# Kernel tuning notes

Hardware: AMD Instinct MI355X
Metric: run time of the kernel (lower is better)

## Reference

```python
import jax, jax.numpy as jnp
import numpy as np

ITEMNUM = 50000
NUM_HEADS = 4
EPS = 1e-8


def _ln(x, g, b):
    m = x.mean(-1, keepdims=True)
    v = ((x - m) ** 2).mean(-1, keepdims=True)
    return (x - m) * jax.lax.rsqrt(v + EPS) * g + b


def _forward(seqs_data, position, seqs, time_emb, pos_table, gate_W, gate_b,
             ln_attn_g, ln_attn_b, qW, qb, kW, kb, vW, vb,
             ln_ffn_g, ln_ffn_b, c1W, c1b, c2W, c2b, last_g, last_b):
    B, L, H = seqs.shape
    nb = qW.shape[0]
    hd = H // NUM_HEADS

    pe = pos_table[position]                      # [B,L,H]
    seqs = seqs + pe
    time = time_emb + pe
    # per-position per-block time gates, [B,L,nb]
    gates = jax.nn.sigmoid(jnp.einsum('blh,nh->bln', time, gate_W) + gate_b)

    keep = (seqs_data != ITEMNUM - 1)[..., None].astype(seqs.dtype)  # [B,L,1]
    seqs = seqs * keep
    tril = jnp.tril(jnp.ones((L, L), dtype=bool))  # causal: keep lower triangle
    neg_inf = jnp.asarray(-jnp.inf, seqs.dtype)
    scale = 1.0 / np.sqrt(hd).astype(np.float32)

    for i in range(nb):
        Q = _ln(seqs, ln_attn_g[i], ln_attn_b[i])
        q = Q @ qW[i].T + qb[i]
        k = time @ kW[i].T + kb[i]
        v = (seqs + time) @ vW[i].T + vb[i]
        # [B,nh,L,hd]
        q = q.reshape(B, L, NUM_HEADS, hd).transpose(0, 2, 1, 3)
        k = k.reshape(B, L, NUM_HEADS, hd).transpose(0, 2, 1, 3)
        v = v.reshape(B, L, NUM_HEADS, hd).transpose(0, 2, 1, 3)
        scores = jnp.einsum('bhqd,bhkd->bhqk', q, k) * scale  # [B,nh,L,L]
        tg = gates[:, :, i]                                   # [B,L]
        gate_mat = tg[:, None, :, None] * tg[:, None, None, :]  # [B,1,L,L] outer product
        scores = jnp.where(tril[None, None], scores * gate_mat, neg_inf)
        attn = jax.nn.softmax(scores, axis=-1)
        out = jnp.einsum('bhqk,bhkd->bhqd', attn, v)
        out = out.transpose(0, 2, 1, 3).reshape(B, L, H)
        x = Q + out
        x = _ln(x, ln_ffn_g[i], ln_ffn_b[i])
        # PointWiseFeedForward: two 1x1 convs == two linears, relu, residual
        h = jax.nn.relu(x @ c1W[i].T + c1b[i])
        seqs = (h @ c2W[i].T + c2b[i] + x) * keep

    return _ln(seqs, last_g, last_b)


def setup_inputs() -> dict:
    key = jax.random.key(0)
    B, L, H, NB, ML = 64, 512, 256, 2, 512
    ks = iter(jax.random.split(key, 32))
    nrm = lambda shape, s=0.05: jax.random.normal(next(ks), shape, jnp.float32) * s
    pos_table = nrm((ML, H), 0.02).at[0].set(0.0)  # padding_idx=0
    inp = {
        'seqs_data': jax.random.randint(next(ks), (B, L), 0, ITEMNUM - 1, jnp.int32),
        'seqs': nrm((B, L, H), 1.0),
        'position': jax.random.randint(next(ks), (B, L), 0, ML, jnp.int32),
        'time_emb': nrm((B, L, H), 1.0),
        'pos_table': pos_table,
        'gate_W': nrm((NB, H)), 'gate_b': jnp.zeros((NB,), jnp.float32),
        'ln_attn_g': jnp.ones((NB, H), jnp.float32), 'ln_attn_b': jnp.zeros((NB, H), jnp.float32),
        'qW': nrm((NB, H, H)), 'qb': jnp.zeros((NB, H), jnp.float32),
        'kW': nrm((NB, H, H)), 'kb': jnp.zeros((NB, H), jnp.float32),
        'vW': nrm((NB, H, H)), 'vb': jnp.zeros((NB, H), jnp.float32),
        'ln_ffn_g': jnp.ones((NB, H), jnp.float32), 'ln_ffn_b': jnp.zeros((NB, H), jnp.float32),
        'c1W': nrm((NB, H, H)), 'c1b': jnp.zeros((NB, H), jnp.float32),
        'c2W': nrm((NB, H, H)), 'c2b': jnp.zeros((NB, H), jnp.float32),
        'last_g': jnp.ones((H,), jnp.float32), 'last_b': jnp.zeros((H,), jnp.float32),
    }
    return inp


def reference(seqs_data, seqs, position, time_emb, pos_table, gate_W, gate_b,
              ln_attn_g, ln_attn_b, qW, qb, kW, kb, vW, vb,
              ln_ffn_g, ln_ffn_b, c1W, c1b, c2W, c2b, last_g, last_b):
    return _forward(seqs_data, position, seqs, time_emb, pos_table, gate_W, gate_b,
                    ln_attn_g, ln_attn_b, qW, qb, kW, kb, vW, vb,
                    ln_ffn_g, ln_ffn_b, c1W, c1b, c2W, c2b, last_g, last_b)
```

## Files before the change

kernel.cpp:

```cpp
#include <hip/hip_runtime.h>
#include <hip/hip_bf16.h>
#include <math.h>

#define NTOK 32768
#define Hdim 256
#define Ldim 512
#define Bdim 64
#define NHEAD 4
#define HD 64
#define PADV 49999

typedef __bf16 bf16x8 __attribute__((ext_vector_type(8)));
typedef __bf16 bf16x4 __attribute__((ext_vector_type(4)));
typedef float  f32x4  __attribute__((ext_vector_type(4)));
typedef unsigned short u16x8 __attribute__((ext_vector_type(8)));

union bf8u { bf16x8 v8; bf16x4 v4[2]; };

__device__ __forceinline__ unsigned short f2bf(float f) {
    unsigned int u = __float_as_uint(f);
    unsigned int r = (u + 0x7fffu + ((u >> 16) & 1u)) >> 16;
    return (unsigned short)r;
}
__device__ __forceinline__ float bf2f(unsigned short u) {
    return __uint_as_float(((unsigned int)u) << 16);
}

__device__ __forceinline__ void gload16(const void* g, void* l) {
    __builtin_amdgcn_global_load_lds((const __attribute__((address_space(1))) unsigned int*)g,
                                     (__attribute__((address_space(3))) unsigned int*)l,
                                     16, 0, 0);
}

__global__ __launch_bounds__(256)
void castw_kernel(const float* __restrict__ q, const float* __restrict__ k,
                  const float* __restrict__ v, const float* __restrict__ c1,
                  const float* __restrict__ c2, unsigned short* __restrict__ dst) {
    const float* srcs[5] = {q, k, v, c1, c2};
    const float* s = srcs[blockIdx.y];
    int idx = blockIdx.x * 1024 + threadIdx.x * 4;
    float4 f = *(const float4*)(s + idx);
    unsigned short* d = dst + (size_t)blockIdx.y * 131072 + idx;
    d[0] = f2bf(f.x); d[1] = f2bf(f.y); d[2] = f2bf(f.z); d[3] = f2bf(f.w);
}

__global__ __launch_bounds__(256)
void prep_ln_kernel(const int* __restrict__ seqs_data, const float* __restrict__ seqs,
                    const int* __restrict__ position, const float* __restrict__ time_emb,
                    const float* __restrict__ pos_table, const float* __restrict__ gate_W,
                    const float* __restrict__ gate_b,
                    const float* __restrict__ lnG, const float* __restrict__ lnB,
                    unsigned short* __restrict__ Tbf,
                    unsigned short* __restrict__ QXbf,
                    unsigned short* __restrict__ VINbf,
                    float* __restrict__ gates, float* __restrict__ keepv) {
    int tok  = blockIdx.x * 4 + (threadIdx.x >> 6);
    int lane = threadIdx.x & 63;
    size_t off = (size_t)tok * Hdim + lane * 4;
    int pos = position[tok];
    float4 pe = *(const float4*)(pos_table + (size_t)pos * Hdim + lane * 4);
    float4 sq = *(const float4*)(seqs + off);
    float4 tm = *(const float4*)(time_emb + off);
    float keep = (seqs_data[tok] != PADV) ? 1.0f : 0.0f;
    float4 t = {tm.x + pe.x, tm.y + pe.y, tm.z + pe.z, tm.w + pe.w};
    float4 s = {(sq.x + pe.x) * keep, (sq.y + pe.y) * keep,
                (sq.z + pe.z) * keep, (sq.w + pe.w) * keep};
    ushort4 tb = {f2bf(t.x), f2bf(t.y), f2bf(t.z), f2bf(t.w)};
    *(ushort4*)(Tbf + off) = tb;
    float4 gw0 = *(const float4*)(gate_W + lane * 4);
    float4 gw1 = *(const float4*)(gate_W + Hdim + lane * 4);
    float r0 = s.x + s.y + s.z + s.w;
    float r1 = s.x * s.x + s.y * s.y + s.z * s.z + s.w * s.w;
    float r2 = t.x * gw0.x + t.y * gw0.y + t.z * gw0.z + t.w * gw0.w;
    float r3 = t.x * gw1.x + t.y * gw1.y + t.z * gw1.z + t.w * gw1.w;
#pragma unroll
    for (int o = 1; o < 64; o <<= 1) {
        r0 += __shfl_xor(r0, o, 64);
        r1 += __shfl_xor(r1, o, 64);
        r2 += __shfl_xor(r2, o, 64);
        r3 += __shfl_xor(r3, o, 64);
    }
    float mean = r0 * (1.0f / Hdim);
    float var  = fmaxf(r1 * (1.0f / Hdim) - mean * mean, 0.0f);
    float rstd = rsqrtf(var + 1e-8f);
    if (lane == 0) {
        gates[(size_t)tok * 2 + 0] = 1.0f / (1.0f + __expf(-(r2 + gate_b[0])));
        gates[(size_t)tok * 2 + 1] = 1.0f / (1.0f + __expf(-(r3 + gate_b[1])));
        keepv[tok] = keep;
    }
    float4 g4 = *(const float4*)(lnG + lane * 4);
    float4 b4 = *(const float4*)(lnB + lane * 4);
    float4 y = {(s.x - mean) * rstd * g4.x + b4.x, (s.y - mean) * rstd * g4.y + b4.y,
                (s.z - mean) * rstd * g4.z + b4.z, (s.w - mean) * rstd * g4.w + b4.w};
    ushort4 yb = {f2bf(y.x), f2bf(y.y), f2bf(y.z), f2bf(y.w)};
    *(ushort4*)(QXbf + off) = yb;
    ushort4 vb = {f2bf(s.x + t.x), f2bf(s.y + t.y), f2bf(s.z + t.z), f2bf(s.w + t.w)};
    *(ushort4*)(VINbf + off) = vb;
}

#define GBM 128
#define GBN 128
#define GBK 64

__device__ __forceinline__ void stage64(const unsigned short* __restrict__ src,
                                        size_t rowBase, __bf16* lds, int tid, int kc) {
#pragma unroll
    for (int it = 0; it < 4; ++it) {
        int c = tid + it * 256;
        int r = c >> 3, sub = c & 7;
        int g = sub ^ (r & 7);
        gload16(src + (rowBase + r) * Hdim + kc + g * 8, lds + c * 8);
    }
}
__device__ __forceinline__ bf16x8 frag64(const __bf16* lds, int r, int g) {
    return *(const bf16x8*)(lds + r * 64 + (g ^ (r & 7)) * 8);
}

__global__ __launch_bounds__(256)
void gemm_qkv_kernel(const unsigned short* __restrict__ QXbf,
                     const unsigned short* __restrict__ Tbf,
                     const unsigned short* __restrict__ VINbf,
                     const unsigned short* __restrict__ qW,
                     const unsigned short* __restrict__ kW,
                     const unsigned short* __restrict__ vW,
                     const float* __restrict__ qb, const float* __restrict__ kb,
                     const float* __restrict__ vb,
                     unsigned short* __restrict__ Qbf,
                     unsigned short* __restrict__ Kbf,
                     unsigned short* __restrict__ VT) {
    __shared__ __align__(16) char smem[128 * 136 * 2];
    __bf16* As = (__bf16*)smem;
    __bf16* Ws = (__bf16*)(smem + 16384);
    __bf16 (*Ct)[136] = (__bf16 (*)[136])smem;
    int z = blockIdx.z;
    const unsigned short* A = (z == 0) ? QXbf : (z == 1) ? Tbf : VINbf;
    const unsigned short* W = (z == 0) ? qW : (z == 1) ? kW : vW;
    const float* bias       = (z == 0) ? qb : (z == 1) ? kb : vb;

    int tid = threadIdx.x, lane = tid & 63, w = tid >> 6;
    int wr = w >> 1, wc = w & 1;
    int m0 = blockIdx.y * GBM, n0 = blockIdx.x * GBN;
    f32x4 acc[4][4];
#pragma unroll
    for (int i = 0; i < 4; ++i)
#pragma unroll
        for (int j = 0; j < 4; ++j) acc[i][j] = (f32x4)(0.0f);
    int colq = lane & 15, kg = lane >> 4;
    for (int kc = 0; kc < Hdim; kc += GBK) {
        __syncthreads();
        stage64(A, m0, As, tid, kc);
        stage64(W, n0, Ws, tid, kc);
        __syncthreads();
        bf16x8 af[4][2], bfr[4][2];
#pragma unroll
        for (int i = 0; i < 4; ++i) {
            int r = wr * 64 + i * 16 + colq;
            af[i][0] = frag64(As, r, kg);
            af[i][1] = frag64(As, r, 4 + kg);
        }
#pragma unroll
        for (int j = 0; j < 4; ++j) {
            int r = wc * 64 + j * 16 + colq;
            bfr[j][0] = frag64(Ws, r, kg);
            bfr[j][1] = frag64(Ws, r, 4 + kg);
        }
#pragma unroll
        for (int i = 0; i < 4; ++i)
#pragma unroll
            for (int j = 0; j < 4; ++j) {
                acc[i][j] = __builtin_amdgcn_mfma_f32_16x16x32_bf16(af[i][0], bfr[j][0], acc[i][j], 0, 0, 0);
                acc[i][j] = __builtin_amdgcn_mfma_f32_16x16x32_bf16(af[i][1], bfr[j][1], acc[i][j], 0, 0, 0);
            }
    }
    int rowq = (lane >> 4) * 4;
    if (z < 2) {
        unsigned short* outBF = (z == 0) ? Qbf : Kbf;
#pragma unroll
        for (int i = 0; i < 4; ++i)
#pragma unroll
            for (int r = 0; r < 4; ++r) {
                int m = m0 + wr * 64 + i * 16 + rowq + r;
#pragma unroll
                for (int j = 0; j < 4; ++j) {
                    int n = n0 + wc * 64 + j * 16 + colq;
                    outBF[(size_t)m * Hdim + n] = f2bf(acc[i][j][r] + bias[n]);
                }
            }
    } else {
        __syncthreads();
#pragma unroll
        for (int i = 0; i < 4; ++i)
#pragma unroll
            for (int r = 0; r < 4; ++r) {
                int ml = wr * 64 + i * 16 + rowq + r;
#pragma unroll
                for (int j = 0; j < 4; ++j) {
                    int nl = wc * 64 + j * 16 + colq;
                    Ct[nl][ml] = (__bf16)(acc[i][j][r] + bias[n0 + nl]);
                }
            }
        __syncthreads();
        int bb = m0 >> 9, l0 = m0 & 511;
#pragma unroll
        for (int it = 0; it < 8; ++it) {
            int c = tid + it * 256;
            int nl = c >> 4;
            int o8 = (c & 15) * 8;
            int n = n0 + nl;
            int hh = n >> 6, dd = n & 63;
            bf16x8 v = *(const bf16x8*)&Ct[nl][o8];
            *(bf16x8*)(VT + ((((size_t)bb * NHEAD + hh) * HD + dd) * Ldim + l0 + o8)) = v;
        }
    }
}

#define FBM 64
#define FFN_LDS (32768 + 32768 + 512)

__device__ __forceinline__ int swz(int r, int g) {
    return (g & 24) | ((g & 7) ^ (r & 7));
}

__device__ __forceinline__ void ffn_stage(const unsigned short* __restrict__ W, int kc,
                                          __bf16* Wst, int tid) {
#pragma unroll
    for (int it = 0; it < 8; ++it) {
        int c = tid + it * 256;
        int r = c >> 3, sub = c & 7;
        int g = sub ^ (r & 7);
        gload16(W + (size_t)r * Hdim + kc + g * 8, Wst + c * 8);
    }
}

__device__ __forceinline__ void ffn_gemm(const unsigned short* __restrict__ W,
                                         const __bf16* Abuf, __bf16* Wst,
                                         int tid, int w, int colq, int kg,
                                         f32x4 acc[4][4]) {
#pragma unroll
    for (int i = 0; i < 4; ++i)
#pragma unroll
        for (int j = 0; j < 4; ++j) acc[i][j] = (f32x4)(0.0f);
    for (int kc = 0; kc < Hdim; kc += 64) {
        __syncthreads();
        bf16x8 af[4][2], bfr[4][2];
#pragma unroll
        for (int i = 0; i < 4; ++i) {
            int r = i * 16 + colq;
            af[i][0] = *(const bf16x8*)(Abuf + r * 256 + ((kc >> 3) | (kg ^ (r & 7))) * 8);
            af[i][1] = *(const bf16x8*)(Abuf + r * 256 + ((kc >> 3) | ((4 + kg) ^ (r & 7))) * 8);
        }
#pragma unroll
        for (int j = 0; j < 4; ++j) {
            int n = w * 64 + j * 16 + colq;
            bfr[j][0] = frag64(Wst, n, kg);
            bfr[j][1] = frag64(Wst, n, 4 + kg);
        }
        __syncthreads();
        if (kc < Hdim - 64) ffn_stage(W, kc + 64, Wst, tid);
#pragma unroll
        for (int i = 0; i < 4; ++i)
#pragma unroll
            for (int j = 0; j < 4; ++j) {
                acc[i][j] = __builtin_amdgcn_mfma_f32_16x16x32_bf16(af[i][0], bfr[j][0], acc[i][j], 0, 0, 0);
                acc[i][j] = __builtin_amdgcn_mfma_f32_16x16x32_bf16(af[i][1], bfr[j][1], acc[i][j], 0, 0, 0);
            }
    }
}

__global__ __launch_bounds__(256, 2)
void ffn_kernel(const unsigned short* __restrict__ Qx,
                const unsigned short* __restrict__ Qa,
                const float* __restrict__ lnG, const float* __restrict__ lnB,
                const unsigned short* __restrict__ c1Wb, const float* __restrict__ c1b,
                const unsigned short* __restrict__ c2Wb, const float* __restrict__ c2b,
                const float* __restrict__ keepv,
                const unsigned short* __restrict__ Tbf,
                const float* __restrict__ oG, const float* __restrict__ oB,
                float* __restrict__ outF,
                unsigned short* __restrict__ QxOut,
                unsigned short* __restrict__ VINout) {
    extern __shared__ __align__(16) char smem[];
    __bf16* Abuf   = (__bf16*)smem;
    __bf16* Wst    = (__bf16*)(smem + 32768);
    float*  statsF = (float*)(smem + 65536);

    int m0  = blockIdx.x * FBM;
    int tid = threadIdx.x, lane = tid & 63, w = tid >> 6;
    int colq = lane & 15, kg = lane >> 4;
    int rowq = kg * 4;

    ffn_stage(c1Wb, 0, Wst, tid);

    u16x8 qvr[8], avr[8];
#pragma unroll
    for (int it = 0; it < 8; ++it) {
        int c = tid + it * 256;
        int r = c >> 5, g = c & 31;
        size_t off = (size_t)(m0 + r) * Hdim + g * 8;
        qvr[it] = *(const u16x8*)(Qx + off);
        avr[it] = *(const u16x8*)(Qa + off);
    }
#pragma unroll
    for (int it = 0; it < 8; ++it) {
        int c = tid + it * 256;
        int r = c >> 5;
        float cs = 0.0f, cq = 0.0f;
#pragma unroll
        for (int j = 0; j < 8; ++j) {
            float x = bf2f(qvr[it][j]) + bf2f(avr[it][j]);
            cs += x; cq += x * x;
        }
#pragma unroll
        for (int o = 1; o < 32; o <<= 1) {
            cs += __shfl_xor(cs, o, 32);
            cq += __shfl_xor(cq, o, 32);
        }
        if ((tid & 31) == 0) { statsF[r * 2] = cs; statsF[r * 2 + 1] = cq; }
    }
    __syncthreads();
    u16x8 xnreg[8];
#pragma unroll
    for (int it = 0; it < 8; ++it) {
        int c = tid + it * 256;
        int r = c >> 5, g = c & 31, col = g * 8;
        float mean = statsF[r * 2] * (1.0f / Hdim);
        float var  = fmaxf(statsF[r * 2 + 1] * (1.0f / Hdim) - mean * mean, 0.0f);
        float rstd = rsqrtf(var + 1e-8f);
        float4 g0 = *(const float4*)(lnG + col), g1 = *(const float4*)(lnG + col + 4);
        float4 b0 = *(const float4*)(lnB + col), b1 = *(const float4*)(lnB + col + 4);
        float gv[8] = {g0.x, g0.y, g0.z, g0.w, g1.x, g1.y, g1.z, g1.w};
        float bv[8] = {b0.x, b0.y, b0.z, b0.w, b1.x, b1.y, b1.z, b1.w};
        u16x8 xn;
#pragma unroll
        for (int j = 0; j < 8; ++j) {
            float x = bf2f(qvr[it][j]) + bf2f(avr[it][j]);
            xn[j] = f2bf((x - mean) * rstd * gv[j] + bv[j]);
        }
        xnreg[it] = xn;
        *(u16x8*)(Abuf + r * 256 + swz(r, g) * 8) = xn;
    }

    f32x4 acc[4][4];
    ffn_gemm(c1Wb, Abuf, Wst, tid, w, colq, kg, acc);
    ffn_stage(c2Wb, 0, Wst, tid);
    float bj[4];
#pragma unroll
    for (int j = 0; j < 4; ++j) bj[j] = c1b[w * 64 + j * 16 + colq];
#pragma unroll
    for (int i = 0; i < 4; ++i)
#pragma unroll
        for (int r = 0; r < 4; ++r) {
            int m = i * 16 + rowq + r;
#pragma unroll
            for (int j = 0; j < 4; ++j) {
                int n = w * 64 + j * 16 + colq;
                float v = fmaxf(acc[i][j][r] + bj[j], 0.0f);
                Abuf[m * 256 + swz(m, n >> 3) * 8 + (n & 7)] = (__bf16)v;
            }
        }

    ffn_gemm(c2Wb, Abuf, Wst, tid, w, colq, kg, acc);
#pragma unroll
    for (int j = 0; j < 4; ++j) bj[j] = c2b[w * 64 + j * 16 + colq];
#pragma unroll
    for (int i = 0; i < 4; ++i)
#pragma unroll
        for (int r = 0; r < 4; ++r) {
            int m = i * 16 + rowq + r;
#pragma unroll
            for (int j = 0; j < 4; ++j) {
                int n = w * 64 + j * 16 + colq;
                Abuf[m * 256 + swz(m, n >> 3) * 8 + (n & 7)] = (__bf16)(acc[i][j][r] + bj[j]);
            }
        }
    __syncthreads();

    u16x8 zvr[8];
#pragma unroll
    for (int it = 0; it < 8; ++it) {
        int c = tid + it * 256;
        int r = c >> 5, g = c & 31;
        zvr[it] = *(const u16x8*)(Abuf + r * 256 + swz(r, g) * 8);
    }
#pragma unroll
    for (int it = 0; it < 8; ++it) {
        int c = tid + it * 256;
        int r = c >> 5;
        float kf = keepv[m0 + r];
        float cs = 0.0f, cq = 0.0f;
#pragma unroll
        for (int j = 0; j < 8; ++j) {
            float s = (bf2f(zvr[it][j]) + bf2f(xnreg[it][j])) * kf;
            cs += s; cq += s * s;
        }
#pragma unroll
        for (int o = 1; o < 32; o <<= 1) {
            cs += __shfl_xor(cs, o, 32);
            cq += __shfl_xor(cq, o, 32);
        }
        if ((tid & 31) == 0) { statsF[r * 2] = cs; statsF[r * 2 + 1] = cq; }
    }
    __syncthreads();
#pragma unroll
    for (int it = 0; it < 8; ++it) {
        int c = tid + it * 256;
        int r = c >> 5, g = c & 31, col = g * 8;
        float kf = keepv[m0 + r];
        float mean = statsF[r * 2] * (1.0f / Hdim);
        float var  = fmaxf(statsF[r * 2 + 1] * (1.0f / Hdim) - mean * mean, 0.0f);
        float rstd = rsqrtf(var + 1e-8f);
        float4 g0 = *(const float4*)(oG + col), g1 = *(const float4*)(oG + col + 4);
        float4 b0 = *(const float4*)(oB + col), b1 = *(const float4*)(oB + col + 4);
        float gv[8] = {g0.x, g0.y, g0.z, g0.w, g1.x, g1.y, g1.z, g1.w};
        float bv[8] = {b0.x, b0.y, b0.z, b0.w, b1.x, b1.y, b1.z, b1.w};
        size_t off = (size_t)(m0 + r) * Hdim + col;
        float y[8], sv[8];
#pragma unroll
        for (int j = 0; j < 8; ++j) {
            sv[j] = (bf2f(zvr[it][j]) + bf2f(xnreg[it][j])) * kf;
            y[j] = (sv[j] - mean) * rstd * gv[j] + bv[j];
        }
        if (outF) {
            float4 o0 = {y[0], y[1], y[2], y[3]};
            float4 o1 = {y[4], y[5], y[6], y[7]};
            *(float4*)(outF + off)     = o0;
            *(float4*)(outF + off + 4) = o1;
        } else {
            u16x8 yb, vb;
            u16x8 tv = *(const u16x8*)(Tbf + off);
#pragma unroll
            for (int j = 0; j < 8; ++j) {
                yb[j] = f2bf(y[j]);
                vb[j] = f2bf(sv[j] + bf2f(tv[j]));
            }
            *(u16x8*)(QxOut + off)  = yb;
            *(u16x8*)(VINout + off) = vb;
        }
    }
}

#define AKS 68
#define AVS 516
#define APS 68
#define ATTN_LDS (512 * AKS * 2 + 64 * AVS * 2 + 192 * APS * 2)
__global__ __launch_bounds__(768, 1)
void attn_mfma_kernel(const unsigned short* __restrict__ Qg,
                      const unsigned short* __restrict__ Kg,
                      const unsigned short* __restrict__ VTg,
                      const float* __restrict__ gates,
                      unsigned short* __restrict__ Ob, int blk) {
    extern __shared__ __align__(16) char smem[];
    __bf16 (*Ks)[AKS]  = (__bf16 (*)[AKS])smem;
    __bf16 (*VTs)[AVS] = (__bf16 (*)[AVS])(smem + 512 * AKS * 2);
    __bf16 (*Ps)[APS]  = (__bf16 (*)[APS])(smem + 512 * AKS * 2 + 64 * AVS * 2);
    int h = blockIdx.x & 3, b = blockIdx.x >> 2;
    int tid = threadIdx.x, lane = tid & 63, w = tid >> 6;
    int colq = lane & 15, grp = lane >> 4;
    int rowq = grp * 4, kq = grp * 8;

    size_t baseK = (size_t)b * Ldim * Hdim + h * HD;
    for (int c = tid; c < 4096; c += 768) {
        int r = c >> 3, o = (c & 7) * 8;
        bf8u u;
        u.v8 = *(const bf16x8*)(Kg + baseK + (size_t)r * Hdim + o);
        *(bf16x4*)&Ks[r][o]     = u.v4[0];
        *(bf16x4*)&Ks[r][o + 4] = u.v4[1];
    }
    size_t baseV = ((size_t)b * NHEAD + h) * HD * Ldim;
    for (int c = tid; c < 4096; c += 768) {
        int d = c >> 6, k = (c & 63) * 8;
        bf8u u;
        u.v8 = *(const bf16x8*)(VTg + baseV + (size_t)d * Ldim + k);
        *(bf16x4*)&VTs[d][k]     = u.v4[0];
        *(bf16x4*)&VTs[d][k + 4] = u.v4[1];
    }
    __syncthreads();

    const float lscale = 0.125f * 1.44269504f;
    int gl[3], ng;
    if (w < 4)      { gl[0] = w;     gl[1] = 8 + w;  gl[2] = 28 + w; ng = 3; }
    else if (w < 8) { gl[0] = w;     gl[1] = 8 + w;  gl[2] = 16 + w; ng = 3; }
    else            { gl[0] = 8 + w; gl[1] = 16 + w; gl[2] = 0;      ng = 2; }

    for (int gi = 0; gi < ng; ++gi) {
        int g = gl[gi];
        int q0 = g * 16;
        size_t qrow = (size_t)(b * Ldim + q0 + colq) * Hdim + h * HD;
        bf16x8 afq0 = *(const bf16x8*)(Qg + qrow + kq);
        bf16x8 afq1 = *(const bf16x8*)(Qg + qrow + 32 + kq);
        float gql[4];
#pragma unroll
        for (int r = 0; r < 4; ++r)
            gql[r] = gates[((size_t)b * Ldim + q0 + rowq + r) * 2 + blk] * lscale;

        float lrun[4] = {0.0f, 0.0f, 0.0f, 0.0f};
        f32x4 accO[4];
#pragma unroll
        for (int jd = 0; jd < 4; ++jd) accO[jd] = (f32x4)(0.0f);

        int nfull = g >> 2;
        for (int kt = 0; kt <= nfull; ++kt) {
            int k0 = kt * 64;
            bool diag = (kt == nfull);
            f32x4 sv[4];
#pragma unroll
            for (int j = 0; j < 4; ++j) sv[j] = (f32x4)(0.0f);
#pragma unroll
            for (int j = 0; j < 4; ++j) {
                int kr = k0 + j * 16 + colq;
                bf8u b0, b1;
                b0.v4[0] = *(const bf16x4*)&Ks[kr][kq];
                b0.v4[1] = *(const bf16x4*)&Ks[kr][kq + 4];
                b1.v4[0] = *(const bf16x4*)&Ks[kr][32 + kq];
                b1.v4[1] = *(const bf16x4*)&Ks[kr][32 + kq + 4];
                sv[j] = __builtin_amdgcn_mfma_f32_16x16x32_bf16(afq0, b0.v8, sv[j], 0, 0, 0);
                sv[j] = __builtin_amdgcn_mfma_f32_16x16x32_bf16(afq1, b1.v8, sv[j], 0, 0, 0);
            }
            float gkv[4];
#pragma unroll
            for (int j = 0; j < 4; ++j)
                gkv[j] = gates[((size_t)b * Ldim + k0 + j * 16 + colq) * 2 + blk];
#pragma unroll
            for (int r = 0; r < 4; ++r) {
                float su = 0.0f;
                float p4[4];
                if (diag) {
                    int qg = q0 + rowq + r;
#pragma unroll
                    for (int j = 0; j < 4; ++j) {
                        float v = sv[j][r] * gql[r] * gkv[j];
                        v = (k0 + j * 16 + colq > qg) ? -1e38f : v;
                        float e = exp2f(v);
                        p4[j] = e;
                        su += e;
                    }
                } else {
#pragma unroll
                    for (int j = 0; j < 4; ++j) {
                        float e = exp2f(sv[j][r] * gql[r] * gkv[j]);
                        p4[j] = e;
                        su += e;
                    }
                }
#pragma unroll
                for (int off = 1; off < 16; off <<= 1)
                    su += __shfl_xor(su, off, 16);
                lrun[r] += su;
#pragma unroll
                for (int j = 0; j < 4; ++j)
                    Ps[w * 16 + rowq + r][j * 16 + colq] = (__bf16)p4[j];
            }
            bf8u a0, a1;
            a0.v4[0] = *(const bf16x4*)&Ps[w * 16 + colq][kq];
            a0.v4[1] = *(const bf16x4*)&Ps[w * 16 + colq][kq + 4];
            a1.v4[0] = *(const bf16x4*)&Ps[w * 16 + colq][32 + kq];
            a1.v4[1] = *(const bf16x4*)&Ps[w * 16 + colq][32 + kq + 4];
#pragma unroll
            for (int jd = 0; jd < 4; ++jd) {
                int vr = jd * 16 + colq;
                bf8u v0, v1;
                v0.v4[0] = *(const bf16x4*)&VTs[vr][k0 + kq];
                v0.v4[1] = *(const bf16x4*)&VTs[vr][k0 + kq + 4];
                v1.v4[0] = *(const bf16x4*)&VTs[vr][k0 + 32 + kq];
                v1.v4[1] = *(const bf16x4*)&VTs[vr][k0 + 32 + kq + 4];
                accO[jd] = __builtin_amdgcn_mfma_f32_16x16x32_bf16(a0.v8, v0.v8, accO[jd], 0, 0, 0);
                accO[jd] = __builtin_amdgcn_mfma_f32_16x16x32_bf16(a1.v8, v1.v8, accO[jd], 0, 0, 0);
            }
        }
#pragma unroll
        for (int r = 0; r < 4; ++r) {
            float inv = 1.0f / lrun[r];
#pragma unroll
            for (int jd = 0; jd < 4; ++jd)
                Ob[(size_t)(b * Ldim + q0 + rowq + r) * Hdim + h * HD + jd * 16 + colq] =
                    f2bf(accO[jd][r] * inv);
        }
    }
}

extern "C" void kernel_launch(void* const* d_in, const int* in_sizes, int n_in,
                              void* d_out, int out_size, void* d_ws, size_t ws_size,
                              hipStream_t stream) {
    const int*   seqs_data = (const int*)d_in[0];
    const float* seqs      = (const float*)d_in[1];
    const int*   position  = (const int*)d_in[2];
    const float* time_emb  = (const float*)d_in[3];
    const float* pos_table = (const float*)d_in[4];
    const float* gate_W    = (const float*)d_in[5];
    const float* gate_b    = (const float*)d_in[6];
    const float* ln_attn_g = (const float*)d_in[7];
    const float* ln_attn_b = (const float*)d_in[8];
    const float* qW        = (const float*)d_in[9];
    const float* qb        = (const float*)d_in[10];
    const float* kW        = (const float*)d_in[11];
    const float* kb        = (const float*)d_in[12];
    const float* vW        = (const float*)d_in[13];
    const float* vb        = (const float*)d_in[14];
    const float* ln_ffn_g  = (const float*)d_in[15];
    const float* ln_ffn_b  = (const float*)d_in[16];
    const float* c1W       = (const float*)d_in[17];
    const float* c1b       = (const float*)d_in[18];
    const float* c2W       = (const float*)d_in[19];
    const float* c2b       = (const float*)d_in[20];
    const float* last_g    = (const float*)d_in[21];
    const float* last_b    = (const float*)d_in[22];

    size_t BUF = (size_t)NTOK * Hdim;
    float* fws = (float*)d_ws;
    float* GATES = fws;
    float* KEEP  = GATES + (size_t)NTOK * 2;
    unsigned short* bws   = (unsigned short*)(KEEP + NTOK);
    unsigned short* Tbf   = bws;
    unsigned short* QXbf  = Tbf + BUF;
    unsigned short* VINbf = QXbf + BUF;
    unsigned short* HIDbf = VINbf + BUF;
    unsigned short* Qbf   = HIDbf + BUF;
    unsigned short* Kbf   = Qbf + BUF;
    unsigned short* VTbf  = Kbf + BUF;
    unsigned short* QAbf  = VTbf + BUF;
    unsigned short* Zbf   = QAbf + BUF;
    unsigned short* Wbf   = Zbf + BUF;
    size_t WB = (size_t)Hdim * Hdim;
    unsigned short* qWbf  = Wbf;
    unsigned short* kWbf  = Wbf + 2 * WB;
    unsigned short* vWbf  = Wbf + 4 * WB;
    unsigned short* c1Wbf = Wbf + 6 * WB;
    unsigned short* c2Wbf = Wbf + 8 * WB;

    castw_kernel<<<dim3(128, 5), 256, 0, stream>>>(qW, kW, vW, c1W, c2W, Wbf);
    prep_ln_kernel<<<NTOK / 4, 256, 0, stream>>>(seqs_data, seqs, position, time_emb,
                                                 pos_table, gate_W, gate_b,
                                                 ln_attn_g, ln_attn_b,
                                                 Tbf, QXbf, VINbf, GATES, KEEP);

    dim3 qkvgrid(Hdim / GBN, NTOK / GBM, 3);
    for (int i = 0; i < 2; ++i) {
        gemm_qkv_kernel<<<qkvgrid, 256, 0, stream>>>(QXbf, Tbf, VINbf,
                                                     qWbf + i * WB, kWbf + i * WB, vWbf + i * WB,
                                                     qb + i * Hdim, kb + i * Hdim, vb + i * Hdim,
                                                     Qbf, Kbf, VTbf);
        attn_mfma_kernel<<<Bdim * NHEAD, 768, ATTN_LDS, stream>>>(Qbf, Kbf, VTbf, GATES, QAbf, i);
        ffn_kernel<<<NTOK / FBM, 256, FFN_LDS, stream>>>(
            QXbf, QAbf,
            ln_ffn_g + i * Hdim, ln_ffn_b + i * Hdim,
            c1Wbf + i * WB, c1b + i * Hdim,
            c2Wbf + i * WB, c2b + i * Hdim,
            KEEP, Tbf,
            (i == 0) ? ln_attn_g + Hdim : last_g,
            (i == 0) ? ln_attn_b + Hdim : last_b,
            (i == 0) ? nullptr : (float*)d_out,
            QXbf, VINbf);
    }
}
```

Before: 357.3 us.

## Stage full FFN weight matrix in LDS and use shuffle-only layernorm stats

The FFN kernel now loads the whole 256x256 bf16 weight matrix (128 KB) into LDS at once instead of streaming 64-column K chunks with per-chunk barriers. The K loop is fully unrolled with no synchronisation inside it. Layernorm statistics come directly from the wave shuffle reduction instead of an LDS round trip and an extra barrier. LDS use grows to about 160 KB per block and the two-blocks-per-CU launch bound is dropped, so occupancy falls to one block per CU and less load latency can be hidden.

```diff
diff --git a/kernel.cpp b/kernel.cpp
--- a/kernel.cpp
+++ b/kernel.cpp
@@ -215,48 +215,48 @@
 }
 
 #define FBM 64
-#define FFN_LDS (32768 + 32768 + 512)
+#define FFN_LDS (32768 + 131072)
 
 __device__ __forceinline__ int swz(int r, int g) {
     return (g & 24) | ((g & 7) ^ (r & 7));
 }
 
-__device__ __forceinline__ void ffn_stage(const unsigned short* __restrict__ W, int kc,
-                                          __bf16* Wst, int tid) {
-#pragma unroll
-    for (int it = 0; it < 8; ++it) {
+__device__ __forceinline__ void ffn_stageW(const unsigned short* __restrict__ W,
+                                           __bf16* Wst, int tid) {
+#pragma unroll
+    for (int it = 0; it < 32; ++it) {
         int c = tid + it * 256;
-        int r = c >> 3, sub = c & 7;
-        int g = sub ^ (r & 7);
-        gload16(W + (size_t)r * Hdim + kc + g * 8, Wst + c * 8);
-    }
-}
-
-__device__ __forceinline__ void ffn_gemm(const unsigned short* __restrict__ W,
-                                         const __bf16* Abuf, __bf16* Wst,
-                                         int tid, int w, int colq, int kg,
-                                         f32x4 acc[4][4]) {
+        int r = c >> 5, s = c & 31;
+        int g = (s & 24) | ((s & 7) ^ (r & 7));
+        gload16(W + (size_t)r * Hdim + g * 8, Wst + c * 8);
+    }
+}
+
+__device__ __forceinline__ bf16x8 fragW(const __bf16* buf, int row, int slot8) {
+    return *(const bf16x8*)(buf + row * 256 + swz(row, slot8) * 8);
+}
+
+__device__ __forceinline__ void ffn_gemm(const __bf16* Abuf, const __bf16* Wst,
+                                         int w, int colq, int kg, f32x4 acc[4][4]) {
 #pragma unroll
     for (int i = 0; i < 4; ++i)
 #pragma unroll
         for (int j = 0; j < 4; ++j) acc[i][j] = (f32x4)(0.0f);
+#pragma unroll
     for (int kc = 0; kc < Hdim; kc += 64) {
-        __syncthreads();
         bf16x8 af[4][2], bfr[4][2];
 #pragma unroll
         for (int i = 0; i < 4; ++i) {
             int r = i * 16 + colq;
-            af[i][0] = *(const bf16x8*)(Abuf + r * 256 + ((kc >> 3) | (kg ^ (r & 7))) * 8);
-            af[i][1] = *(const bf16x8*)(Abuf + r * 256 + ((kc >> 3) | ((4 + kg) ^ (r & 7))) * 8);
+            af[i][0] = fragW(Abuf, r, (kc >> 3) + kg);
+            af[i][1] = fragW(Abuf, r, (kc >> 3) + 4 + kg);
         }
 #pragma unroll
         for (int j = 0; j < 4; ++j) {
             int n = w * 64 + j * 16 + colq;
-            bfr[j][0] = frag64(Wst, n, kg);
-            bfr[j][1] = frag64(Wst, n, 4 + kg);
-        }
-        __syncthreads();
-        if (kc < Hdim - 64) ffn_stage(W, kc + 64, Wst, tid);
+            bfr[j][0] = fragW(Wst, n, (kc >> 3) + kg);
+            bfr[j][1] = fragW(Wst, n, (kc >> 3) + 4 + kg);
+        }
 #pragma unroll
         for (int i = 0; i < 4; ++i)
 #pragma unroll
@@ -267,7 +267,7 @@
     }
 }
 
-__global__ __launch_bounds__(256, 2)
+__global__ __launch_bounds__(256)
 void ffn_kernel(const unsigned short* __restrict__ Qx,
                 const unsigned short* __restrict__ Qa,
                 const float* __restrict__ lnG, const float* __restrict__ lnB,
@@ -280,16 +280,15 @@
                 unsigned short* __restrict__ QxOut,
                 unsigned short* __restrict__ VINout) {
     extern __shared__ __align__(16) char smem[];
-    __bf16* Abuf   = (__bf16*)smem;
-    __bf16* Wst    = (__bf16*)(smem + 32768);
-    float*  statsF = (float*)(smem + 65536);
+    __bf16* Abuf = (__bf16*)smem;
+    __bf16* Wst  = (__bf16*)(smem + 32768);
 
     int m0  = blockIdx.x * FBM;
     int tid = threadIdx.x, lane = tid & 63, w = tid >> 6;
     int colq = lane & 15, kg = lane >> 4;
     int rowq = kg * 4;
 
-    ffn_stage(c1Wb, 0, Wst, tid);
+    ffn_stageW(c1Wb, Wst, tid);
 
     u16x8 qvr[8], avr[8];
 #pragma unroll
@@ -300,31 +299,25 @@
         qvr[it] = *(const u16x8*)(Qx + off);
         avr[it] = *(const u16x8*)(Qa + off);
     }
+    u16x8 xnreg[8];
 #pragma unroll
     for (int it = 0; it < 8; ++it) {
         int c = tid + it * 256;
-        int r = c >> 5;
+        int r = c >> 5, g = c & 31, col = g * 8;
+        float x[8];
         float cs = 0.0f, cq = 0.0f;
 #pragma unroll
         for (int j = 0; j < 8; ++j) {
-            float x = bf2f(qvr[it][j]) + bf2f(avr[it][j]);
-            cs += x; cq += x * x;
+            x[j] = bf2f(qvr[it][j]) + bf2f(avr[it][j]);
+            cs += x[j]; cq += x[j] * x[j];
         }
 #pragma unroll
         for (int o = 1; o < 32; o <<= 1) {
             cs += __shfl_xor(cs, o, 32);
             cq += __shfl_xor(cq, o, 32);
         }
-        if ((tid & 31) == 0) { statsF[r * 2] = cs; statsF[r * 2 + 1] = cq; }
-    }
-    __syncthreads();
-    u16x8 xnreg[8];
-#pragma unroll
-    for (int it = 0; it < 8; ++it) {
-        int c = tid + it * 256;
-        int r = c >> 5, g = c & 31, col = g * 8;
-        float mean = statsF[r * 2] * (1.0f / Hdim);
-        float var  = fmaxf(statsF[r * 2 + 1] * (1.0f / Hdim) - mean * mean, 0.0f);
+        float mean = cs * (1.0f / Hdim);
+        float var  = fmaxf(cq * (1.0f / Hdim) - mean * mean, 0.0f);
         float rstd = rsqrtf(var + 1e-8f);
         float4 g0 = *(const float4*)(lnG + col), g1 = *(const float4*)(lnG + col + 4);
         float4 b0 = *(const float4*)(lnB + col), b1 = *(const float4*)(lnB + col + 4);
@@ -332,17 +325,17 @@
         float bv[8] = {b0.x, b0.y, b0.z, b0.w, b1.x, b1.y, b1.z, b1.w};
         u16x8 xn;
 #pragma unroll
-        for (int j = 0; j < 8; ++j) {
-            float x = bf2f(qvr[it][j]) + bf2f(avr[it][j]);
-            xn[j] = f2bf((x - mean) * rstd * gv[j] + bv[j]);
-        }
+        for (int j = 0; j < 8; ++j)
+            xn[j] = f2bf((x[j] - mean) * rstd * gv[j] + bv[j]);
         xnreg[it] = xn;
         *(u16x8*)(Abuf + r * 256 + swz(r, g) * 8) = xn;
     }
+    __syncthreads();
 
     f32x4 acc[4][4];
-    ffn_gemm(c1Wb, Abuf, Wst, tid, w, colq, kg, acc);
-    ffn_stage(c2Wb, 0, Wst, tid);
+    ffn_gemm(Abuf, Wst, w, colq, kg, acc);
+    __syncthreads();
+    ffn_stageW(c2Wb, Wst, tid);
     float bj[4];
 #pragma unroll
     for (int j = 0; j < 4; ++j) bj[j] = c1b[w * 64 + j * 16 + colq];
@@ -358,8 +351,10 @@
                 Abuf[m * 256 + swz(m, n >> 3) * 8 + (n & 7)] = (__bf16)v;
             }
         }
-
-    ffn_gemm(c2Wb, Abuf, Wst, tid, w, colq, kg, acc);
+    __syncthreads();
+
+    ffn_gemm(Abuf, Wst, w, colq, kg, acc);
+    __syncthreads();
 #pragma unroll
     for (int j = 0; j < 4; ++j) bj[j] = c2b[w * 64 + j * 16 + colq];
 #pragma unroll
@@ -385,41 +380,32 @@
 #pragma unroll
     for (int it = 0; it < 8; ++it) {
         int c = tid + it * 256;
-        int r = c >> 5;
+        int r = c >> 5, g = c & 31, col = g * 8;
         float kf = keepv[m0 + r];
+        float sv[8];
         float cs = 0.0f, cq = 0.0f;
 #pragma unroll
         for (int j = 0; j < 8; ++j) {
-            float s = (bf2f(zvr[it][j]) + bf2f(xnreg[it][j])) * kf;
-            cs += s; cq += s * s;
+            sv[j] = (bf2f(zvr[it][j]) + bf2f(xnreg[it][j])) * kf;
+            cs += sv[j]; cq += sv[j] * sv[j];
         }
 #pragma unroll
         for (int o = 1; o < 32; o <<= 1) {
             cs += __shfl_xor(cs, o, 32);
             cq += __shfl_xor(cq, o, 32);
         }
-        if ((tid & 31) == 0) { statsF[r * 2] = cs; statsF[r * 2 + 1] = cq; }
-    }
-    __syncthreads();
-#pragma unroll
-    for (int it = 0; it < 8; ++it) {
-        int c = tid + it * 256;
-        int r = c >> 5, g = c & 31, col = g * 8;
-        float kf = keepv[m0 + r];
-        float mean = statsF[r * 2] * (1.0f / Hdim);
-        float var  = fmaxf(statsF[r * 2 + 1] * (1.0f / Hdim) - mean * mean, 0.0f);
+        float mean = cs * (1.0f / Hdim);
+        float var  = fmaxf(cq * (1.0f / Hdim) - mean * mean, 0.0f);
         float rstd = rsqrtf(var + 1e-8f);
         float4 g0 = *(const float4*)(oG + col), g1 = *(const float4*)(oG + col + 4);
         float4 b0 = *(const float4*)(oB + col), b1 = *(const float4*)(oB + col + 4);
         float gv[8] = {g0.x, g0.y, g0.z, g0.w, g1.x, g1.y, g1.z, g1.w};
         float bv[8] = {b0.x, b0.y, b0.z, b0.w, b1.x, b1.y, b1.z, b1.w};
         size_t off = (size_t)(m0 + r) * Hdim + col;
-        float y[8], sv[8];
-#pragma unroll
-        for (int j = 0; j < 8; ++j) {
-            sv[j] = (bf2f(zvr[it][j]) + bf2f(xnreg[it][j])) * kf;
+        float y[8];
+#pragma unroll
+        for (int j = 0; j < 8; ++j)
             y[j] = (sv[j] - mean) * rstd * gv[j] + bv[j];
-        }
         if (outF) {
             float4 o0 = {y[0], y[1], y[2], y[3]};
             float4 o1 = {y[4], y[5], y[6], y[7]};
```

Result: slower. 367.7 us (+2.9%).
